# Kernel optimization log

Measured on AMD Instinct MI355X. Metric: run time of the kernel, lower is better.

The kernel has to match this reference:

```python
import jax, jax.numpy as jnp
import numpy as np

SEQ_LEN = 8192
HIDDEN = 1024
NUM_SPANS = 4096
MAX_W = 32  # max span width (end - start + 1 <= MAX_W)
NEG_INF = -1e9


def setup_inputs() -> dict:
    key = jax.random.key(0)
    k_emb, k_s, k_w, k_aw = jax.random.split(key, 4)
    embeddings = jax.random.normal(k_emb, (1, SEQ_LEN, HIDDEN), dtype=jnp.float32)
    starts = jax.random.randint(k_s, (NUM_SPANS,), 0, SEQ_LEN - MAX_W, dtype=jnp.int32)
    widths = jax.random.randint(k_w, (NUM_SPANS,), 0, MAX_W, dtype=jnp.int32)  # width-1 in [0, MAX_W-1]
    ends = starts + widths
    attn_w = jax.random.normal(k_aw, (HIDDEN,), dtype=jnp.float32) * (HIDDEN ** -0.5)
    attn_b = jnp.zeros((), dtype=jnp.float32)
    return {"embeddings": embeddings, "starts": starts, "ends": ends,
            "attn_w": attn_w, "attn_b": attn_b}


def reference(embeddings, starts, ends, attn_w, attn_b):
    emb = embeddings[0]  # (S_len, H) -- original code indexes batch 0
    # Padded span positions: (num_spans, MAX_W)
    pos = starts[:, None] + jnp.arange(MAX_W, dtype=starts.dtype)[None, :]
    mask = pos <= ends[:, None]
    pos_c = jnp.minimum(pos, SEQ_LEN - 1)
    span_emb = emb[pos_c]  # (num_spans, MAX_W, H) gather
    # Linear(H -> 1) attention scores, masked softmax over span positions
    scores = jnp.einsum("swh,h->sw", span_emb, attn_w) + attn_b
    scores = jnp.where(mask, scores, NEG_INF)
    weights = jax.nn.softmax(scores, axis=1)
    attn_out = jnp.einsum("sw,swh->sh", weights, span_emb)
    start_emb = emb[starts]  # (num_spans, H)
    end_emb = emb[ends]
    return jnp.concatenate([start_emb, end_emb, attn_out], axis=-1)  # (num_spans, 3H)
```

## Files before the change

kernel.cpp:

```cpp
#include <hip/hip_runtime.h>
#include <math.h>

#define SEQ_LEN   8192
#define HIDDEN    1024
#define NUM_SPANS 4096
#define MAX_W     32
#define NBLK      (NUM_SPANS / 4)
#define NXCD      8

typedef float f4v __attribute__((ext_vector_type(4)));

__device__ __forceinline__ float dot4(float4 a, float4 b) {
    return a.x * b.x + a.y * b.y + a.z * b.z + a.w * b.w;
}

__device__ __forceinline__ void nt_store4(float4* p, float4 v) {
    f4v x = { v.x, v.y, v.z, v.w };
    __builtin_nontemporal_store(x, (f4v*)p);
}

__global__ __launch_bounds__(1024) void sort_spans_kernel(
    const int* __restrict__ starts,
    int* __restrict__ perm)
{
    __shared__ int hist[1024];
    __shared__ int base[1024];
    __shared__ int wsum[16];

    const int tid  = threadIdx.x;
    const int lane = tid & 63;
    const int wid  = tid >> 6;

    hist[tid] = 0;
    __syncthreads();

    #pragma unroll
    for (int i = tid; i < NUM_SPANS; i += 1024)
        atomicAdd(&hist[starts[i] >> 3], 1);
    __syncthreads();

    const int v = hist[tid];
    int sc = v;
    #pragma unroll
    for (int off = 1; off < 64; off <<= 1) {
        const int t = __shfl_up(sc, off, 64);
        if (lane >= off) sc += t;
    }
    if (lane == 63) wsum[wid] = sc;
    __syncthreads();
    if (wid == 0 && lane < 16) {
        int ws = wsum[lane];
        #pragma unroll
        for (int off = 1; off < 16; off <<= 1) {
            const int t = __shfl_up(ws, off, 64);
            if (lane >= off) ws += t;
        }
        wsum[lane] = ws;
    }
    __syncthreads();
    const int waveOff = (wid == 0) ? 0 : wsum[wid - 1];
    base[tid] = waveOff + sc - v;
    __syncthreads();

    hist[tid] = 0;
    __syncthreads();

    #pragma unroll
    for (int i = tid; i < NUM_SPANS; i += 1024) {
        const int b   = starts[i] >> 3;
        const int pos = base[b] + atomicAdd(&hist[b], 1);
        perm[pos] = i;
    }
}

__global__ __launch_bounds__(256, 4) void span_repr_kernel(
    const float* __restrict__ emb,
    const int* __restrict__ starts,
    const int* __restrict__ ends,
    const float* __restrict__ attn_w,
    const float* __restrict__ attn_b,
    const int* __restrict__ perm,
    float* __restrict__ out)
{
    const int tid = threadIdx.x;
    const int w2  = tid >> 6;
    const int c   = tid & 63;

    const int slot = (blockIdx.x & (NXCD - 1)) * (NBLK / NXCD) + (blockIdx.x >> 3);
    const int s    = perm[(slot << 2) + w2];

    const int start = starts[s];
    const int wmax  = ends[s] - start;
    const float bias = attn_b[0];

    const float4* __restrict__ embr = (const float4*)emb + (size_t)start * 256;

    const float4* __restrict__ wv4 = (const float4*)attn_w;
    const float4 wv0 = wv4[c];
    const float4 wv1 = wv4[c + 64];
    const float4 wv2 = wv4[c + 128];
    const float4 wv3 = wv4[c + 192];

    float4* __restrict__ out4 = (float4*)(out + (size_t)s * (3 * HIDDEN));

    float4 v0 = embr[c];
    float4 v1 = embr[c + 64];
    float4 v2 = embr[c + 128];
    float4 v3 = embr[c + 192];

    nt_store4(&out4[c],       v0);
    nt_store4(&out4[c + 64],  v1);
    nt_store4(&out4[c + 128], v2);
    nt_store4(&out4[c + 192], v3);

    float4 a0 = make_float4(0.f, 0.f, 0.f, 0.f);
    float4 a1 = make_float4(0.f, 0.f, 0.f, 0.f);
    float4 a2 = make_float4(0.f, 0.f, 0.f, 0.f);
    float4 a3 = make_float4(0.f, 0.f, 0.f, 0.f);
    float m = -INFINITY;
    float l = 0.0f;

    for (int r = 0; r <= wmax; ++r) {
        const float4* __restrict__ nr = embr + (size_t)min(r + 1, wmax) * 256;
        float4 n0 = nr[c];
        float4 n1 = nr[c + 64];
        float4 n2 = nr[c + 128];
        float4 n3 = nr[c + 192];
        __builtin_amdgcn_sched_barrier(0);

        float p = dot4(v0, wv0) + dot4(v1, wv1) + dot4(v2, wv2) + dot4(v3, wv3);
        #pragma unroll
        for (int off = 32; off > 0; off >>= 1)
            p += __shfl_xor(p, off, 64);
        const float sc = p + bias;

        if (sc > m) {
            const float alpha = __expf(m - sc);
            a0.x *= alpha; a0.y *= alpha; a0.z *= alpha; a0.w *= alpha;
            a1.x *= alpha; a1.y *= alpha; a1.z *= alpha; a1.w *= alpha;
            a2.x *= alpha; a2.y *= alpha; a2.z *= alpha; a2.w *= alpha;
            a3.x *= alpha; a3.y *= alpha; a3.z *= alpha; a3.w *= alpha;
            l *= alpha;
            m = sc;
        }
        const float e = __expf(sc - m);
        l += e;
        a0.x += e * v0.x; a0.y += e * v0.y; a0.z += e * v0.z; a0.w += e * v0.w;
        a1.x += e * v1.x; a1.y += e * v1.y; a1.z += e * v1.z; a1.w += e * v1.w;
        a2.x += e * v2.x; a2.y += e * v2.y; a2.z += e * v2.z; a2.w += e * v2.w;
        a3.x += e * v3.x; a3.y += e * v3.y; a3.z += e * v3.z; a3.w += e * v3.w;

        v0 = n0; v1 = n1; v2 = n2; v3 = n3;
    }

    nt_store4(&out4[256 + c],       v0);
    nt_store4(&out4[256 + c + 64],  v1);
    nt_store4(&out4[256 + c + 128], v2);
    nt_store4(&out4[256 + c + 192], v3);

    const float inv = 1.0f / l;
    nt_store4(&out4[512 + c],
              make_float4(a0.x * inv, a0.y * inv, a0.z * inv, a0.w * inv));
    nt_store4(&out4[512 + c + 64],
              make_float4(a1.x * inv, a1.y * inv, a1.z * inv, a1.w * inv));
    nt_store4(&out4[512 + c + 128],
              make_float4(a2.x * inv, a2.y * inv, a2.z * inv, a2.w * inv));
    nt_store4(&out4[512 + c + 192],
              make_float4(a3.x * inv, a3.y * inv, a3.z * inv, a3.w * inv));
}

extern "C" void kernel_launch(void* const* d_in, const int* in_sizes, int n_in,
                              void* d_out, int out_size, void* d_ws, size_t ws_size,
                              hipStream_t stream) {
    const float* emb    = (const float*)d_in[0];
    const int*   starts = (const int*)d_in[1];
    const int*   ends   = (const int*)d_in[2];
    const float* attn_w = (const float*)d_in[3];
    const float* attn_b = (const float*)d_in[4];
    float* out = (float*)d_out;

    int* perm = (int*)d_ws;

    sort_spans_kernel<<<1, 1024, 0, stream>>>(starts, perm);
    span_repr_kernel<<<NBLK, 256, 0, stream>>>(emb, starts, ends, attn_w, attn_b, perm, out);
}
```

Before: 113.0 us.

## Precompute per-row attention scores and split hidden dim across two waves per span

Attention scores are now computed once per sequence row in a prep kernel, merged with the span sort, instead of being recomputed for every span position. The main kernel loads the precomputed scores, runs a wave-level softmax, and accumulates weighted rows without online rescaling. Each span is split across two waves that each handle half the hidden dimension, doubling the block count and raising occupancy. The prep pass adds a full read of the embedding matrix (about 32MB) in exchange for removing the per-position dot products and shuffle reductions.

```diff
diff --git a/kernel.cpp b/kernel.cpp
--- a/kernel.cpp
+++ b/kernel.cpp
@@ -5,7 +5,7 @@
 #define HIDDEN    1024
 #define NUM_SPANS 4096
 #define MAX_W     32
-#define NBLK      (NUM_SPANS / 4)
+#define NBLK2     2048
 #define NXCD      8
 
 typedef float f4v __attribute__((ext_vector_type(4)));
@@ -19,17 +19,38 @@
     __builtin_nontemporal_store(x, (f4v*)p);
 }
 
-__global__ __launch_bounds__(1024) void sort_spans_kernel(
+__global__ __launch_bounds__(1024) void prep_kernel(
     const int* __restrict__ starts,
-    int* __restrict__ perm)
+    const float* __restrict__ emb,
+    const float* __restrict__ attn_w,
+    const float* __restrict__ attn_b,
+    int* __restrict__ perm,
+    float* __restrict__ scores)
 {
+    const int tid  = threadIdx.x;
+    const int lane = tid & 63;
+    const int wid  = tid >> 6;
+
+    if (blockIdx.x < 512) {
+        const int row = (blockIdx.x << 4) + wid;
+        const float4* __restrict__ wv4 = (const float4*)attn_w;
+        const float4 wv0 = wv4[lane];
+        const float4 wv1 = wv4[lane + 64];
+        const float4 wv2 = wv4[lane + 128];
+        const float4 wv3 = wv4[lane + 192];
+        const float4* __restrict__ rp = (const float4*)emb + (size_t)row * 256;
+        float p = dot4(rp[lane],       wv0) + dot4(rp[lane + 64],  wv1)
+                + dot4(rp[lane + 128], wv2) + dot4(rp[lane + 192], wv3);
+        #pragma unroll
+        for (int off = 32; off > 0; off >>= 1)
+            p += __shfl_xor(p, off, 64);
+        if (lane == 0) scores[row] = p + attn_b[0];
+        return;
+    }
+
     __shared__ int hist[1024];
     __shared__ int base[1024];
     __shared__ int wsum[16];
-
-    const int tid  = threadIdx.x;
-    const int lane = tid & 63;
-    const int wid  = tid >> 6;
 
     hist[tid] = 0;
     __syncthreads();
@@ -73,100 +94,71 @@
     }
 }
 
-__global__ __launch_bounds__(256, 4) void span_repr_kernel(
+__global__ __launch_bounds__(256, 8) void span_repr_kernel(
     const float* __restrict__ emb,
     const int* __restrict__ starts,
     const int* __restrict__ ends,
-    const float* __restrict__ attn_w,
-    const float* __restrict__ attn_b,
     const int* __restrict__ perm,
+    const float* __restrict__ scores,
     float* __restrict__ out)
 {
     const int tid = threadIdx.x;
     const int w2  = tid >> 6;
     const int c   = tid & 63;
 
-    const int slot = (blockIdx.x & (NXCD - 1)) * (NBLK / NXCD) + (blockIdx.x >> 3);
-    const int s    = perm[(slot << 2) + w2];
+    const int slot = (blockIdx.x & (NXCD - 1)) * (NBLK2 / NXCD) + (blockIdx.x >> 3);
+    const int s    = perm[(slot << 1) + (w2 >> 1)];
+    const int h    = w2 & 1;
 
     const int start = starts[s];
     const int wmax  = ends[s] - start;
-    const float bias = attn_b[0];
 
-    const float4* __restrict__ embr = (const float4*)emb + (size_t)start * 256;
+    const float sc = (c <= wmax) ? scores[start + c] : -INFINITY;
+    float mx = sc;
+    #pragma unroll
+    for (int off = 32; off > 0; off >>= 1)
+        mx = fmaxf(mx, __shfl_xor(mx, off, 64));
+    const float e = (c <= wmax) ? __expf(sc - mx) : 0.0f;
+    float sum = e;
+    #pragma unroll
+    for (int off = 32; off > 0; off >>= 1)
+        sum += __shfl_xor(sum, off, 64);
+    const float wt = e / sum;
 
-    const float4* __restrict__ wv4 = (const float4*)attn_w;
-    const float4 wv0 = wv4[c];
-    const float4 wv1 = wv4[c + 64];
-    const float4 wv2 = wv4[c + 128];
-    const float4 wv3 = wv4[c + 192];
-
-    float4* __restrict__ out4 = (float4*)(out + (size_t)s * (3 * HIDDEN));
+    const float4* __restrict__ embr = (const float4*)emb + (size_t)start * 256 + (h << 7);
+    float4* __restrict__ out4 = (float4*)(out + (size_t)s * (3 * HIDDEN)) + (h << 7);
 
     float4 v0 = embr[c];
     float4 v1 = embr[c + 64];
-    float4 v2 = embr[c + 128];
-    float4 v3 = embr[c + 192];
+    nt_store4(&out4[c],      v0);
+    nt_store4(&out4[c + 64], v1);
 
-    nt_store4(&out4[c],       v0);
-    nt_store4(&out4[c + 64],  v1);
-    nt_store4(&out4[c + 128], v2);
-    nt_store4(&out4[c + 192], v3);
+    const float w0 = __shfl(wt, 0, 64);
+    float4 a0 = make_float4(w0 * v0.x, w0 * v0.y, w0 * v0.z, w0 * v0.w);
+    float4 a1 = make_float4(w0 * v1.x, w0 * v1.y, w0 * v1.z, w0 * v1.w);
 
-    float4 a0 = make_float4(0.f, 0.f, 0.f, 0.f);
-    float4 a1 = make_float4(0.f, 0.f, 0.f, 0.f);
-    float4 a2 = make_float4(0.f, 0.f, 0.f, 0.f);
-    float4 a3 = make_float4(0.f, 0.f, 0.f, 0.f);
-    float m = -INFINITY;
-    float l = 0.0f;
+    const float4* nr = embr + (size_t)min(1, wmax) * 256;
+    float4 p0 = nr[c];
+    float4 p1 = nr[c + 64];
 
-    for (int r = 0; r <= wmax; ++r) {
-        const float4* __restrict__ nr = embr + (size_t)min(r + 1, wmax) * 256;
-        float4 n0 = nr[c];
-        float4 n1 = nr[c + 64];
-        float4 n2 = nr[c + 128];
-        float4 n3 = nr[c + 192];
+    for (int r = 1; r <= wmax; ++r) {
+        const float4* __restrict__ xr = embr + (size_t)min(r + 1, wmax) * 256;
+        float4 n0 = xr[c];
+        float4 n1 = xr[c + 64];
         __builtin_amdgcn_sched_barrier(0);
 
-        float p = dot4(v0, wv0) + dot4(v1, wv1) + dot4(v2, wv2) + dot4(v3, wv3);
-        #pragma unroll
-        for (int off = 32; off > 0; off >>= 1)
-            p += __shfl_xor(p, off, 64);
-        const float sc = p + bias;
+        const float wr = __shfl(wt, r, 64);
+        a0.x += wr * p0.x; a0.y += wr * p0.y; a0.z += wr * p0.z; a0.w += wr * p0.w;
+        a1.x += wr * p1.x; a1.y += wr * p1.y; a1.z += wr * p1.z; a1.w += wr * p1.w;
 
-        if (sc > m) {
-            const float alpha = __expf(m - sc);
-            a0.x *= alpha; a0.y *= alpha; a0.z *= alpha; a0.w *= alpha;
-            a1.x *= alpha; a1.y *= alpha; a1.z *= alpha; a1.w *= alpha;
-            a2.x *= alpha; a2.y *= alpha; a2.z *= alpha; a2.w *= alpha;
-            a3.x *= alpha; a3.y *= alpha; a3.z *= alpha; a3.w *= alpha;
-            l *= alpha;
-            m = sc;
-        }
-        const float e = __expf(sc - m);
-        l += e;
-        a0.x += e * v0.x; a0.y += e * v0.y; a0.z += e * v0.z; a0.w += e * v0.w;
-        a1.x += e * v1.x; a1.y += e * v1.y; a1.z += e * v1.z; a1.w += e * v1.w;
-        a2.x += e * v2.x; a2.y += e * v2.y; a2.z += e * v2.z; a2.w += e * v2.w;
-        a3.x += e * v3.x; a3.y += e * v3.y; a3.z += e * v3.z; a3.w += e * v3.w;
-
-        v0 = n0; v1 = n1; v2 = n2; v3 = n3;
+        p0 = n0; p1 = n1;
     }
 
-    nt_store4(&out4[256 + c],       v0);
-    nt_store4(&out4[256 + c + 64],  v1);
-    nt_store4(&out4[256 + c + 128], v2);
-    nt_store4(&out4[256 + c + 192], v3);
+    nt_store4(&out4[256 + c],      p0);
+    nt_store4(&out4[256 + c + 64], p1);
 
-    const float inv = 1.0f / l;
-    nt_store4(&out4[512 + c],
-              make_float4(a0.x * inv, a0.y * inv, a0.z * inv, a0.w * inv));
-    nt_store4(&out4[512 + c + 64],
-              make_float4(a1.x * inv, a1.y * inv, a1.z * inv, a1.w * inv));
-    nt_store4(&out4[512 + c + 128],
-              make_float4(a2.x * inv, a2.y * inv, a2.z * inv, a2.w * inv));
-    nt_store4(&out4[512 + c + 192],
-              make_float4(a3.x * inv, a3.y * inv, a3.z * inv, a3.w * inv));
+    nt_store4(&out4[512 + c],      a0);
+    nt_store4(&out4[512 + c + 64], a1);
 }
 
 extern "C" void kernel_launch(void* const* d_in, const int* in_sizes, int n_in,
@@ -179,8 +171,9 @@
     const float* attn_b = (const float*)d_in[4];
     float* out = (float*)d_out;
 
-    int* perm = (int*)d_ws;
+    int*   perm   = (int*)d_ws;
+    float* scores = (float*)((int*)d_ws + NUM_SPANS);
 
-    sort_spans_kernel<<<1, 1024, 0, stream>>>(starts, perm);
-    span_repr_kernel<<<NBLK, 256, 0, stream>>>(emb, starts, ends, attn_w, attn_b, perm, out);
+    prep_kernel<<<513, 1024, 0, stream>>>(starts, emb, attn_w, attn_b, perm, scores);
+    span_repr_kernel<<<NBLK2, 256, 0, stream>>>(emb, starts, ends, perm, scores, out);
 }
```

Result: no change. 111.6 us (-1.2%).
